# Kernel tuning notes

Measured on AMD Instinct MI355X. Metric: run time of the kernel, lower is better.

## Reference

```python
import jax, jax.numpy as jnp
import numpy as np

DIM = 768
NUM_HEADS = 12
HEAD_DIM = DIM // NUM_HEADS
HIDDEN = int(DIM * 0.5)  # 384, per Block: hidden_features = int(dim * 0.5)
SCALE = HEAD_DIM ** 0.5  # NOTE: source multiplies by sqrt(head_dim) (qk_scale=None path)


def setup_inputs() -> dict:
    key = jax.random.key(0)
    ks = jax.random.split(key, 10)
    s = 0.02
    return {
        "x": jax.random.normal(ks[0], (8, 1024, DIM), dtype=jnp.float32),
        "ln1_w": jnp.ones((DIM,), jnp.float32),
        "ln1_b": jnp.zeros((DIM,), jnp.float32),
        "ln2_w": jnp.ones((DIM,), jnp.float32),
        "ln2_b": jnp.zeros((DIM,), jnp.float32),
        "w_qkv": jax.random.normal(ks[1], (DIM, 3 * DIM), jnp.float32) * s,  # no bias (qkv_bias=None)
        "w_proj": jax.random.normal(ks[2], (DIM, DIM), jnp.float32) * s,    # no bias (qkv_bias=None)
        "w_fc1": jax.random.normal(ks[3], (DIM, HIDDEN), jnp.float32) * s,
        "b_fc1": jnp.zeros((HIDDEN,), jnp.float32),
        "w_fc2": jax.random.normal(ks[4], (HIDDEN, DIM), jnp.float32) * s,
        "b_fc2": jnp.zeros((DIM,), jnp.float32),
    }


def _layernorm(x, w, b, eps=1e-5):
    mu = jnp.mean(x, axis=-1, keepdims=True)
    var = jnp.mean(jnp.square(x - mu), axis=-1, keepdims=True)
    return (x - mu) * jax.lax.rsqrt(var + eps) * w + b


def reference(x, ln1_w, ln1_b, ln2_w, ln2_b, w_qkv, w_proj, w_fc1, b_fc1, w_fc2, b_fc2):
    B, N, C = x.shape
    # --- attention branch (pre-norm) ---
    h = _layernorm(x, ln1_w, ln1_b)
    qkv = h @ w_qkv  # [B,N,3C]
    qkv = qkv.reshape(B, N, 3, NUM_HEADS, HEAD_DIM)
    q = jnp.transpose(qkv[:, :, 0], (0, 2, 1, 3))  # [B,H,N,D]
    k = jnp.transpose(qkv[:, :, 1], (0, 2, 1, 3))
    v = jnp.transpose(qkv[:, :, 2], (0, 2, 1, 3))
    attn = jnp.einsum("bhnd,bhmd->bhnm", q, k) * SCALE
    attn = jax.nn.softmax(attn, axis=-1)
    out = jnp.einsum("bhnm,bhmd->bhnd", attn, v)
    out = jnp.transpose(out, (0, 2, 1, 3)).reshape(B, N, C)
    x = x + out @ w_proj
    # --- MLP branch (pre-norm) ---
    h = _layernorm(x, ln2_w, ln2_b)
    h = jax.nn.gelu(h @ w_fc1 + b_fc1, approximate=False)
    x = x + (h @ w_fc2 + b_fc2)
    return x
```

## Files before the change

### kernel.cpp

```cpp
#include <hip/hip_runtime.h>
#include <hip/hip_bf16.h>
#include <math.h>

#define DIM 768
#define NHEAD 12
#define HD 64
#define HIDDEN 384
#define BATCH 8
#define SEQ 1024
#define ROWS (BATCH*SEQ)
#define CHUNKB 4
#define CHUNKR (CHUNKB*SEQ)

typedef short bf16x8 __attribute__((ext_vector_type(8)));
typedef short bf16x4 __attribute__((ext_vector_type(4)));
typedef float f32x4 __attribute__((ext_vector_type(4)));
typedef unsigned short u16;
typedef unsigned int u32;

__device__ __forceinline__ u16 f2bs(float f) {
    unsigned int u = __float_as_uint(f);
    unsigned int r = (u + 0x7FFFu + ((u >> 16) & 1u)) >> 16;
    return (u16)r;
}

__device__ __forceinline__ u32 packbf2(float a, float b) {
    __hip_bfloat162 h = __float22bfloat162_rn(make_float2(a, b));
    u32 r;
    __builtin_memcpy(&r, &h, 4);
    return r;
}

__device__ __forceinline__ float fexp2(float x) {
    return __builtin_amdgcn_exp2f(x);
}

__device__ __forceinline__ void gld16(const u16* g, u16* l) {
    __builtin_amdgcn_global_load_lds(
        (const __attribute__((address_space(1))) unsigned int*)g,
        (__attribute__((address_space(3))) unsigned int*)l, 16, 0, 0);
}

__global__ __launch_bounds__(256) void wtrans4(const float* __restrict__ W0, u16* __restrict__ T0,
                                               const float* __restrict__ W1, u16* __restrict__ T1,
                                               const float* __restrict__ W2, u16* __restrict__ T2,
                                               const float* __restrict__ W3, u16* __restrict__ T3) {
    __shared__ float tile[32][33];
    int id = blockIdx.x;
    const float* W; u16* T; int K, N, nt;
    if (id < 1728)      {            W = W0; T = T0; K = 768; N = 2304; nt = 72; }
    else if (id < 2304) { id -= 1728; W = W1; T = T1; K = 768; N = 768;  nt = 24; }
    else if (id < 2592) { id -= 2304; W = W2; T = T2; K = 768; N = 384;  nt = 12; }
    else                { id -= 2592; W = W3; T = T3; K = 384; N = 768;  nt = 24; }
    int n0 = (id % nt) * 32, k0 = (id / nt) * 32;
    int tx = threadIdx.x & 31, ty = threadIdx.x >> 5;
#pragma unroll
    for (int i = 0; i < 4; i++)
        tile[ty + i * 8][tx] = W[(long)(k0 + ty + i * 8) * N + n0 + tx];
    __syncthreads();
#pragma unroll
    for (int i = 0; i < 4; i++)
        T[(long)(n0 + ty + i * 8) * K + k0 + tx] = f2bs(tile[tx][ty + i * 8]);
}

__global__ __launch_bounds__(256) void lnorm(const float* __restrict__ X,
                                             const float* __restrict__ w,
                                             const float* __restrict__ b,
                                             u16* __restrict__ Y) {
    int row = blockIdx.x;
    const float* xr = X + (long)row * DIM;
    int t = threadIdx.x;
    float v0 = xr[t], v1 = xr[t + 256], v2 = xr[t + 512];
    float s = v0 + v1 + v2;
    float s2 = v0 * v0 + v1 * v1 + v2 * v2;
    for (int off = 1; off < 64; off <<= 1) {
        s  += __shfl_xor(s,  off, 64);
        s2 += __shfl_xor(s2, off, 64);
    }
    __shared__ float ss[4], ss2[4];
    int wid = t >> 6;
    if ((t & 63) == 0) { ss[wid] = s; ss2[wid] = s2; }
    __syncthreads();
    s  = ss[0] + ss[1] + ss[2] + ss[3];
    s2 = ss2[0] + ss2[1] + ss2[2] + ss2[3];
    float mu = s * (1.0f / DIM);
    float var = s2 * (1.0f / DIM) - mu * mu;
    float rstd = rsqrtf(var + 1e-5f);
    u16* yr = Y + (long)row * DIM;
    yr[t]       = f2bs((v0 - mu) * rstd * w[t]       + b[t]);
    yr[t + 256] = f2bs((v1 - mu) * rstd * w[t + 256] + b[t + 256]);
    yr[t + 512] = f2bs((v2 - mu) * rstd * w[t + 512] + b[t + 512]);
}

template <int BM, int BN, int EPI>
__global__ __launch_bounds__(256) void gemm_bt(const u16* __restrict__ A,
                                               const u16* __restrict__ Bt,
                                               int M, int N, int K, int nblk,
                                               u16* __restrict__ Cb,
                                               float* __restrict__ Cf,
                                               const float* __restrict__ resid,
                                               const float* __restrict__ bias) {
    constexpr int MB = BM / 32, NB = BN / 32;
    __shared__ u16 As[BM * 64];
    __shared__ u16 Bs[BN * 64];
    int lin = blockIdx.x;
    int cpx = gridDim.x >> 3;
    int swz = (lin & 7) * cpx + (lin >> 3);
    int m0 = (swz / nblk) * BM;
    int n0 = (swz % nblk) * BN;
    int t = threadIdx.x;
    int lane = t & 63, w = t >> 6;
    int quad = lane >> 4, l16 = lane & 15;
    int wr = w >> 1, wc = w & 1;
    int lr = lane >> 3, lc = lane & 7;
    int sc = (lc ^ lr) * 8;
    int x7 = l16 & 7;

    f32x4 acc[MB][NB];
#pragma unroll
    for (int mb = 0; mb < MB; mb++)
#pragma unroll
        for (int nb = 0; nb < NB; nb++) acc[mb][nb] = (f32x4){0.f, 0.f, 0.f, 0.f};

    for (int kt = 0; kt < K; kt += 64) {
        __syncthreads();
#pragma unroll
        for (int i = 0; i < BM / 32; i++) {
            int rb = i * 32 + w * 8;
            gld16(&A[(long)(m0 + rb + lr) * K + kt + sc], &As[rb * 64]);
        }
#pragma unroll
        for (int i = 0; i < BN / 32; i++) {
            int rb = i * 32 + w * 8;
            gld16(&Bt[(long)(n0 + rb + lr) * K + kt + sc], &Bs[rb * 64]);
        }
        __syncthreads();
#pragma unroll
        for (int kh = 0; kh < 2; kh++) {
            bf16x8 af[MB], bfr[NB];
#pragma unroll
            for (int mb = 0; mb < MB; mb++)
                af[mb] = *(const bf16x8*)&As[(wr * (BM / 2) + mb * 16 + l16) * 64 +
                                             (((kh * 4 + quad) ^ x7) * 8)];
#pragma unroll
            for (int nb = 0; nb < NB; nb++)
                bfr[nb] = *(const bf16x8*)&Bs[(wc * (BN / 2) + nb * 16 + l16) * 64 +
                                              (((kh * 4 + quad) ^ x7) * 8)];
#pragma unroll
            for (int mb = 0; mb < MB; mb++)
#pragma unroll
                for (int nb = 0; nb < NB; nb++)
                    acc[mb][nb] = __builtin_amdgcn_mfma_f32_16x16x32_bf16(af[mb], bfr[nb], acc[mb][nb], 0, 0, 0);
        }
    }

    int mbase = m0 + wr * (BM / 2), nbase = n0 + wc * (BN / 2);
#pragma unroll
    for (int mb = 0; mb < MB; mb++)
#pragma unroll
        for (int nb = 0; nb < NB; nb++) {
            int r0 = mbase + mb * 16 + quad * 4;
            int c = nbase + nb * 16 + l16;
#pragma unroll
            for (int r = 0; r < 4; r++) {
                float v = acc[mb][nb][r];
                long idx = (long)(r0 + r) * N + c;
                if (EPI == 0) {
                    Cb[idx] = f2bs(v);
                } else if (EPI == 1) {
                    Cf[idx] = resid[idx] + v;
                } else if (EPI == 2) {
                    float xg = v + bias[c];
                    Cb[idx] = f2bs(xg * 0.5f * (1.0f + erff(xg * 0.70710678118f)));
                } else {
                    Cf[idx] = resid[idx] + v + bias[c];
                }
            }
        }
}

__global__ __launch_bounds__(512, 6) void attn(const u16* __restrict__ QKV, u16* __restrict__ O) {
    __shared__ u16 Ks[2][64 * 64];
    __shared__ u16 Vs[2][64 * 72];
    int lin = blockIdx.x;
    int cpx = gridDim.x >> 3;
    int l = (lin & 7) * cpx + (lin >> 3);
    int q0 = (l & 7) * 128;
    int hb = l >> 3;
    int h = hb % NHEAD;
    int b = hb / NHEAD;
    int t = threadIdx.x;
    int lane = t & 63, w = t >> 6;
    int quad = lane >> 4, l16 = lane & 15;
    int x7 = l16 & 7;

    const long rs = 3 * DIM;
    const u16* base = QKV + (long)b * SEQ * rs;

    bf16x8 qf0, qf1;
    {
        int qrow = q0 + w * 16 + l16;
        qf0 = *(const bf16x8*)&base[(long)qrow * rs + h * 64 + quad * 8];
        qf1 = *(const bf16x8*)&base[(long)qrow * rs + h * 64 + 32 + quad * 8];
    }

    f32x4 o[4];
#pragma unroll
    for (int dt = 0; dt < 4; dt++) o[dt] = (f32x4){0.f, 0.f, 0.f, 0.f};
    float m_run = -1e30f;
    float l_run = 0.f;
    const float L2E8 = 11.54156032f;

    int lr = lane >> 3, lc = lane & 7;
    int sc = (lc ^ lr) * 8;
    const u16* kA = &base[(long)(w * 8 + lr) * rs + DIM + h * 64 + sc];
    int vc = t & 31, vo = t >> 5;
    const u16* vptr = &base[(long)(2 * vc) * rs + 2 * DIM + h * 64 + vo * 4];
    const long kstep = (long)64 * rs;

    bf16x4 vp0, vp1;
    gld16(kA, &Ks[0][(w * 8) * 64]);
    kA += kstep;
    vp0 = *(const bf16x4*)&vptr[0];
    vp1 = *(const bf16x4*)&vptr[rs];
    vptr += kstep;
#pragma unroll
    for (int j = 0; j < 4; j++) {
        u32 pk = (u32)(u16)vp0[j] | ((u32)(u16)vp1[j] << 16);
        *(u32*)&Vs[0][(vo * 4 + j) * 72 + 2 * vc] = pk;
    }
    vp0 = *(const bf16x4*)&vptr[0];
    vp1 = *(const bf16x4*)&vptr[rs];
    vptr += kstep;
    __syncthreads();

    for (int it = 0; it < SEQ / 64; it++) {
        int cur = it & 1;
        if (it < SEQ / 64 - 1) {
            int nb = cur ^ 1;
            gld16(kA, &Ks[nb][(w * 8) * 64]);
            kA += kstep;
#pragma unroll
            for (int j = 0; j < 4; j++) {
                u32 pk = (u32)(u16)vp0[j] | ((u32)(u16)vp1[j] << 16);
                *(u32*)&Vs[nb][(vo * 4 + j) * 72 + 2 * vc] = pk;
            }
            if (it < SEQ / 64 - 2) {
                vp0 = *(const bf16x4*)&vptr[0];
                vp1 = *(const bf16x4*)&vptr[rs];
                vptr += kstep;
            }
        }

        f32x4 s[4];
#pragma unroll
        for (int jb = 0; jb < 4; jb++) {
            int row = jb * 16 + l16;
            bf16x8 kf0 = *(const bf16x8*)&Ks[cur][row * 64 + ((quad ^ x7) * 8)];
            bf16x8 kf1 = *(const bf16x8*)&Ks[cur][row * 64 + (((4 + quad) ^ x7) * 8)];
            f32x4 z = (f32x4){0.f, 0.f, 0.f, 0.f};
            z = __builtin_amdgcn_mfma_f32_16x16x32_bf16(kf0, qf0, z, 0, 0, 0);
            z = __builtin_amdgcn_mfma_f32_16x16x32_bf16(kf1, qf1, z, 0, 0, 0);
            s[jb] = z;
        }

        f32x4 mx = __builtin_elementwise_max(__builtin_elementwise_max(s[0], s[1]),
                                             __builtin_elementwise_max(s[2], s[3]));
        float m1 = fmaxf(fmaxf(mx[0], mx[1]), fmaxf(mx[2], mx[3]));
        m1 = fmaxf(m1, __shfl_xor(m1, 16, 64));
        m1 = fmaxf(m1, __shfl_xor(m1, 32, 64));

        float mn = m_run;
        int resc = __any(m1 > mn + 8.0f);
        if (resc) mn = fmaxf(mn, m1);
        float mn8 = mn * L2E8;
        f32x4 cmul = {L2E8, L2E8, L2E8, L2E8};
        f32x4 cadd = {-mn8, -mn8, -mn8, -mn8};
#pragma unroll
        for (int jb = 0; jb < 4; jb++) {
            f32x4 e = s[jb] * cmul + cadd;
            e[0] = fexp2(e[0]); e[1] = fexp2(e[1]);
            e[2] = fexp2(e[2]); e[3] = fexp2(e[3]);
            s[jb] = e;
        }
        f32x4 sv = (s[0] + s[1]) + (s[2] + s[3]);
        float rsum = (sv[0] + sv[1]) + (sv[2] + sv[3]);
        rsum += __shfl_xor(rsum, 16, 64);
        rsum += __shfl_xor(rsum, 32, 64);

        if (resc) {
            float alpha = fexp2((m_run - mn) * L2E8);
            m_run = mn;
            float a0 = __shfl(alpha, quad * 4 + 0, 16);
            float a1 = __shfl(alpha, quad * 4 + 1, 16);
            float a2 = __shfl(alpha, quad * 4 + 2, 16);
            float a3 = __shfl(alpha, quad * 4 + 3, 16);
#pragma unroll
            for (int dt = 0; dt < 4; dt++) {
                o[dt][0] *= a0; o[dt][1] *= a1;
                o[dt][2] *= a2; o[dt][3] *= a3;
            }
            l_run = l_run * alpha + rsum;
        } else {
            l_run += rsum;
        }

#pragma unroll
        for (int jp = 0; jp < 2; jp++) {
            int jb0 = 2 * jp, jb1 = 2 * jp + 1;
            union { u32 u[4]; bf16x8 v; } pa;
            pa.u[0] = packbf2(s[jb0][0], s[jb0][1]);
            pa.u[1] = packbf2(s[jb0][2], s[jb0][3]);
            pa.u[2] = packbf2(s[jb1][0], s[jb1][1]);
            pa.u[3] = packbf2(s[jb1][2], s[jb1][3]);
#pragma unroll
            for (int dt = 0; dt < 4; dt++) {
                union { bf16x4 h[2]; bf16x8 v; } vb;
                vb.h[0] = *(const bf16x4*)&Vs[cur][(dt * 16 + l16) * 72 + jb0 * 16 + quad * 4];
                vb.h[1] = *(const bf16x4*)&Vs[cur][(dt * 16 + l16) * 72 + jb1 * 16 + quad * 4];
                o[dt] = __builtin_amdgcn_mfma_f32_16x16x32_bf16(pa.v, vb.v, o[dt], 0, 0, 0);
            }
        }

        if (it < SEQ / 64 - 1) __syncthreads();
    }

    {
        float l0 = __builtin_amdgcn_rcpf(__shfl(l_run, quad * 4 + 0, 16));
        float l1 = __builtin_amdgcn_rcpf(__shfl(l_run, quad * 4 + 1, 16));
        float l2 = __builtin_amdgcn_rcpf(__shfl(l_run, quad * 4 + 2, 16));
        float l3 = __builtin_amdgcn_rcpf(__shfl(l_run, quad * 4 + 3, 16));
        u16* orow = O + ((long)(b * SEQ + q0 + w * 16)) * DIM + h * 64;
#pragma unroll
        for (int dt = 0; dt < 4; dt++) {
            u32 p01 = packbf2(o[dt][0] * l0, o[dt][1] * l1);
            u32 p23 = packbf2(o[dt][2] * l2, o[dt][3] * l3);
            int cidx = dt * 16 + l16;
            orow[(long)(quad * 4 + 0) * DIM + cidx] = (u16)p01;
            orow[(long)(quad * 4 + 1) * DIM + cidx] = (u16)(p01 >> 16);
            orow[(long)(quad * 4 + 2) * DIM + cidx] = (u16)p23;
            orow[(long)(quad * 4 + 3) * DIM + cidx] = (u16)(p23 >> 16);
        }
    }
}

extern "C" void kernel_launch(void* const* d_in, const int* in_sizes, int n_in,
                              void* d_out, int out_size, void* d_ws, size_t ws_size,
                              hipStream_t stream) {
    const float* x     = (const float*)d_in[0];
    const float* ln1w  = (const float*)d_in[1];
    const float* ln1b  = (const float*)d_in[2];
    const float* ln2w  = (const float*)d_in[3];
    const float* ln2b  = (const float*)d_in[4];
    const float* wqkv  = (const float*)d_in[5];
    const float* wproj = (const float*)d_in[6];
    const float* wfc1  = (const float*)d_in[7];
    const float* bfc1  = (const float*)d_in[8];
    const float* wfc2  = (const float*)d_in[9];
    const float* bfc2  = (const float*)d_in[10];
    float* out = (float*)d_out;

    char* ws = (char*)d_ws;
    size_t off = 0;
    auto alloc = [&](size_t bytes) {
        void* p = ws + off;
        off = (off + bytes + 255) & ~(size_t)255;
        return p;
    };
    u16* wt_qkv  = (u16*)alloc((size_t)3 * DIM * DIM * 2);
    u16* wt_proj = (u16*)alloc((size_t)DIM * DIM * 2);
    u16* wt_fc1  = (u16*)alloc((size_t)HIDDEN * DIM * 2);
    u16* wt_fc2  = (u16*)alloc((size_t)DIM * HIDDEN * 2);
    u16* hbuf    = (u16*)alloc((size_t)ROWS * DIM * 2);
    u16* gbuf    = (u16*)alloc((size_t)ROWS * HIDDEN * 2);
    size_t qkv_bytes = (size_t)ROWS * 3 * DIM * 2;
    u16* qkvfull = (off + qkv_bytes + 1024 <= ws_size) ? (u16*)alloc(qkv_bytes) : nullptr;

    wtrans4<<<2880, 256, 0, stream>>>(wqkv, wt_qkv, wproj, wt_proj,
                                      wfc1, wt_fc1, wfc2, wt_fc2);

    lnorm<<<ROWS, 256, 0, stream>>>(x, ln1w, ln1b, hbuf);

    if (qkvfull) {
        gemm_bt<128, 128, 0><<<(3 * DIM / 128) * (ROWS / 128), 256, 0, stream>>>(
            hbuf, wt_qkv, ROWS, 3 * DIM, DIM, 3 * DIM / 128, qkvfull, nullptr, nullptr, nullptr);
        attn<<<(SEQ / 128) * NHEAD * BATCH, 512, 0, stream>>>(qkvfull, hbuf);
    } else {
        u16* qd = (u16*)d_out;
        for (int c = 0; c < ROWS / CHUNKR; c++) {
            const u16* hA = hbuf + (size_t)c * CHUNKR * DIM;
            gemm_bt<128, 128, 0><<<(3 * DIM / 128) * (CHUNKR / 128), 256, 0, stream>>>(
                hA, wt_qkv, CHUNKR, 3 * DIM, DIM, 3 * DIM / 128, qd, nullptr, nullptr, nullptr);
            attn<<<(SEQ / 128) * NHEAD * CHUNKB, 512, 0, stream>>>(
                qd, hbuf + (size_t)c * CHUNKR * DIM);
        }
    }

    gemm_bt<128, 64, 1><<<(DIM / 64) * (ROWS / 128), 256, 0, stream>>>(
        hbuf, wt_proj, ROWS, DIM, DIM, DIM / 64, nullptr, out, x, nullptr);

    lnorm<<<ROWS, 256, 0, stream>>>(out, ln2w, ln2b, hbuf);

    gemm_bt<64, 64, 2><<<(HIDDEN / 64) * (ROWS / 64), 256, 0, stream>>>(
        hbuf, wt_fc1, ROWS, HIDDEN, DIM, HIDDEN / 64, gbuf, nullptr, nullptr, bfc1);

    gemm_bt<128, 64, 3><<<(DIM / 64) * (ROWS / 128), 256, 0, stream>>>(
        gbuf, wt_fc2, ROWS, DIM, HIDDEN, DIM / 64, nullptr, out, out, bfc2);
}
```

Measured before the change: 240.6 us.

## Merge weight transpose with first layernorm and store residual stream in bf16

Result: faster. 235.7 us (-2.0%).

```diff
diff --git a/kernel.cpp b/kernel.cpp
--- a/kernel.cpp
+++ b/kernel.cpp
@@ -24,6 +24,10 @@
     return (u16)r;
 }
 
+__device__ __forceinline__ float bs2f(u16 v) {
+    return __uint_as_float((u32)v << 16);
+}
+
 __device__ __forceinline__ u32 packbf2(float a, float b) {
     __hip_bfloat162 h = __float22bfloat162_rn(make_float2(a, b));
     u32 r;
@@ -41,19 +45,49 @@
         (__attribute__((address_space(3))) unsigned int*)l, 16, 0, 0);
 }
 
-__global__ __launch_bounds__(256) void wtrans4(const float* __restrict__ W0, u16* __restrict__ T0,
-                                               const float* __restrict__ W1, u16* __restrict__ T1,
-                                               const float* __restrict__ W2, u16* __restrict__ T2,
-                                               const float* __restrict__ W3, u16* __restrict__ T3) {
+__global__ __launch_bounds__(256) void prep(const float* __restrict__ X,
+                                            const float* __restrict__ lw,
+                                            const float* __restrict__ lb,
+                                            u16* __restrict__ Y,
+                                            const float* __restrict__ W0, u16* __restrict__ T0,
+                                            const float* __restrict__ W1, u16* __restrict__ T1,
+                                            const float* __restrict__ W2, u16* __restrict__ T2,
+                                            const float* __restrict__ W3, u16* __restrict__ T3) {
     __shared__ float tile[32][33];
+    __shared__ float ss[4], ss2[4];
     int id = blockIdx.x;
+    int t = threadIdx.x;
+    if (id < ROWS) {
+        const float* xr = X + (long)id * DIM;
+        float v0 = xr[t], v1 = xr[t + 256], v2 = xr[t + 512];
+        float s = v0 + v1 + v2;
+        float s2 = v0 * v0 + v1 * v1 + v2 * v2;
+        for (int off = 1; off < 64; off <<= 1) {
+            s  += __shfl_xor(s,  off, 64);
+            s2 += __shfl_xor(s2, off, 64);
+        }
+        int wid = t >> 6;
+        if ((t & 63) == 0) { ss[wid] = s; ss2[wid] = s2; }
+        __syncthreads();
+        s  = ss[0] + ss[1] + ss[2] + ss[3];
+        s2 = ss2[0] + ss2[1] + ss2[2] + ss2[3];
+        float mu = s * (1.0f / DIM);
+        float var = s2 * (1.0f / DIM) - mu * mu;
+        float rstd = rsqrtf(var + 1e-5f);
+        u16* yr = Y + (long)id * DIM;
+        yr[t]       = f2bs((v0 - mu) * rstd * lw[t]       + lb[t]);
+        yr[t + 256] = f2bs((v1 - mu) * rstd * lw[t + 256] + lb[t + 256]);
+        yr[t + 512] = f2bs((v2 - mu) * rstd * lw[t + 512] + lb[t + 512]);
+        return;
+    }
+    id -= ROWS;
     const float* W; u16* T; int K, N, nt;
     if (id < 1728)      {            W = W0; T = T0; K = 768; N = 2304; nt = 72; }
     else if (id < 2304) { id -= 1728; W = W1; T = T1; K = 768; N = 768;  nt = 24; }
     else if (id < 2592) { id -= 2304; W = W2; T = T2; K = 768; N = 384;  nt = 12; }
     else                { id -= 2592; W = W3; T = T3; K = 384; N = 768;  nt = 24; }
     int n0 = (id % nt) * 32, k0 = (id / nt) * 32;
-    int tx = threadIdx.x & 31, ty = threadIdx.x >> 5;
+    int tx = t & 31, ty = t >> 5;
 #pragma unroll
     for (int i = 0; i < 4; i++)
         tile[ty + i * 8][tx] = W[(long)(k0 + ty + i * 8) * N + n0 + tx];
@@ -63,14 +97,14 @@
         T[(long)(n0 + ty + i * 8) * K + k0 + tx] = f2bs(tile[tx][ty + i * 8]);
 }
 
-__global__ __launch_bounds__(256) void lnorm(const float* __restrict__ X,
-                                             const float* __restrict__ w,
-                                             const float* __restrict__ b,
-                                             u16* __restrict__ Y) {
+__global__ __launch_bounds__(256) void lnorm_b(const u16* __restrict__ X,
+                                               const float* __restrict__ w,
+                                               const float* __restrict__ b,
+                                               u16* __restrict__ Y) {
     int row = blockIdx.x;
-    const float* xr = X + (long)row * DIM;
+    const u16* xr = X + (long)row * DIM;
     int t = threadIdx.x;
-    float v0 = xr[t], v1 = xr[t + 256], v2 = xr[t + 512];
+    float v0 = bs2f(xr[t]), v1 = bs2f(xr[t + 256]), v2 = bs2f(xr[t + 512]);
     float s = v0 + v1 + v2;
     float s2 = v0 * v0 + v1 * v1 + v2 * v2;
     for (int off = 1; off < 64; off <<= 1) {
@@ -99,6 +133,7 @@
                                                u16* __restrict__ Cb,
                                                float* __restrict__ Cf,
                                                const float* __restrict__ resid,
+                                               const u16* __restrict__ residb,
                                                const float* __restrict__ bias) {
     constexpr int MB = BM / 32, NB = BN / 32;
     __shared__ u16 As[BM * 64];
@@ -167,13 +202,13 @@
                 long idx = (long)(r0 + r) * N + c;
                 if (EPI == 0) {
                     Cb[idx] = f2bs(v);
-                } else if (EPI == 1) {
-                    Cf[idx] = resid[idx] + v;
                 } else if (EPI == 2) {
                     float xg = v + bias[c];
                     Cb[idx] = f2bs(xg * 0.5f * (1.0f + erff(xg * 0.70710678118f)));
+                } else if (EPI == 4) {
+                    Cb[idx] = f2bs(resid[idx] + v);
                 } else {
-                    Cf[idx] = resid[idx] + v + bias[c];
+                    Cf[idx] = bs2f(residb[idx]) + v + bias[c];
                 }
             }
         }
@@ -373,37 +408,37 @@
     u16* wt_fc2  = (u16*)alloc((size_t)DIM * HIDDEN * 2);
     u16* hbuf    = (u16*)alloc((size_t)ROWS * DIM * 2);
     u16* gbuf    = (u16*)alloc((size_t)ROWS * HIDDEN * 2);
+    u16* hbuf2   = (u16*)alloc((size_t)ROWS * DIM * 2);
     size_t qkv_bytes = (size_t)ROWS * 3 * DIM * 2;
     u16* qkvfull = (off + qkv_bytes + 1024 <= ws_size) ? (u16*)alloc(qkv_bytes) : nullptr;
 
-    wtrans4<<<2880, 256, 0, stream>>>(wqkv, wt_qkv, wproj, wt_proj,
-                                      wfc1, wt_fc1, wfc2, wt_fc2);
-
-    lnorm<<<ROWS, 256, 0, stream>>>(x, ln1w, ln1b, hbuf);
+    prep<<<ROWS + 2880, 256, 0, stream>>>(x, ln1w, ln1b, hbuf,
+                                          wqkv, wt_qkv, wproj, wt_proj,
+                                          wfc1, wt_fc1, wfc2, wt_fc2);
 
     if (qkvfull) {
         gemm_bt<128, 128, 0><<<(3 * DIM / 128) * (ROWS / 128), 256, 0, stream>>>(
-            hbuf, wt_qkv, ROWS, 3 * DIM, DIM, 3 * DIM / 128, qkvfull, nullptr, nullptr, nullptr);
+            hbuf, wt_qkv, ROWS, 3 * DIM, DIM, 3 * DIM / 128, qkvfull, nullptr, nullptr, nullptr, nullptr);
         attn<<<(SEQ / 128) * NHEAD * BATCH, 512, 0, stream>>>(qkvfull, hbuf);
     } else {
         u16* qd = (u16*)d_out;
         for (int c = 0; c < ROWS / CHUNKR; c++) {
             const u16* hA = hbuf + (size_t)c * CHUNKR * DIM;
             gemm_bt<128, 128, 0><<<(3 * DIM / 128) * (CHUNKR / 128), 256, 0, stream>>>(
-                hA, wt_qkv, CHUNKR, 3 * DIM, DIM, 3 * DIM / 128, qd, nullptr, nullptr, nullptr);
+                hA, wt_qkv, CHUNKR, 3 * DIM, DIM, 3 * DIM / 128, qd, nullptr, nullptr, nullptr, nullptr);
             attn<<<(SEQ / 128) * NHEAD * CHUNKB, 512, 0, stream>>>(
                 qd, hbuf + (size_t)c * CHUNKR * DIM);
         }
     }
 
-    gemm_bt<128, 64, 1><<<(DIM / 64) * (ROWS / 128), 256, 0, stream>>>(
-        hbuf, wt_proj, ROWS, DIM, DIM, DIM / 64, nullptr, out, x, nullptr);
-
-    lnorm<<<ROWS, 256, 0, stream>>>(out, ln2w, ln2b, hbuf);
+    gemm_bt<128, 64, 4><<<(DIM / 64) * (ROWS / 128), 256, 0, stream>>>(
+        hbuf, wt_proj, ROWS, DIM, DIM, DIM / 64, hbuf2, nullptr, x, nullptr, nullptr);
+
+    lnorm_b<<<ROWS, 256, 0, stream>>>(hbuf2, ln2w, ln2b, hbuf);
 
     gemm_bt<64, 64, 2><<<(HIDDEN / 64) * (ROWS / 64), 256, 0, stream>>>(
-        hbuf, wt_fc1, ROWS, HIDDEN, DIM, HIDDEN / 64, gbuf, nullptr, nullptr, bfc1);
-
-    gemm_bt<128, 64, 3><<<(DIM / 64) * (ROWS / 128), 256, 0, stream>>>(
-        gbuf, wt_fc2, ROWS, DIM, HIDDEN, DIM / 64, nullptr, out, out, bfc2);
-}
+        hbuf, wt_fc1, ROWS, HIDDEN, DIM, HIDDEN / 64, gbuf, nullptr, nullptr, nullptr, bfc1);
+
+    gemm_bt<128, 64, 5><<<(DIM / 64) * (ROWS / 128), 256, 0, stream>>>(
+        gbuf, wt_fc2, ROWS, DIM, HIDDEN, DIM / 64, nullptr, out, nullptr, hbuf2, bfc2);
+}
```
